# Optimization experiments

Hardware: AMD Instinct MI355X
Metric: run time of the kernel (lower is better)

The kernel has to match this reference:

```python
import jax, jax.numpy as jnp
import numpy as np

B, T, F, H = 512, 64, 256, 1024


def _uniform(key, shape, fan_in):
    stv = 1.0 / np.sqrt(fan_in)
    return jax.random.uniform(key, shape, jnp.float32, -stv, stv)


def setup_inputs() -> dict:
    key = jax.random.key(0)
    ks = jax.random.split(key, 20)
    x = jax.random.normal(ks[0], (B, T, F), jnp.float32)
    mask = (jax.random.uniform(ks[1], (B, T, F)) < 0.8).astype(jnp.float32)
    deltas = jax.random.uniform(ks[2], (B, T, F), jnp.float32) * 5.0
    h0 = jnp.zeros((B, H), jnp.float32)
    return {
        "x": x, "mask": mask, "deltas": deltas, "h0": h0,
        # temp_decay_h: Decay(F -> H), non-diag
        "Wdh": _uniform(ks[3], (H, F), F), "bdh": _uniform(ks[4], (H,), F),
        # temp_decay_x: Decay(F -> F), diag (weight masked with identity)
        "Wdx": _uniform(ks[5], (F, F), F), "bdx": _uniform(ks[6], (F,), F),
        # hist: Linear(H -> F)
        "Wh": _uniform(ks[7], (F, H), H), "bh": _uniform(ks[8], (F,), H),
        "Wfr": _uniform(ks[9], (F, F), F), "bfr": _uniform(ks[10], (F,), F),
        # weight_combine: Linear(2F -> F)
        "Wwc": _uniform(ks[11], (F, 2 * F), 2 * F), "bwc": _uniform(ks[12], (F,), 2 * F),
        # GRUCell(2F, H)
        "Wih": _uniform(ks[13], (3 * H, 2 * F), 2 * F), "bih": _uniform(ks[14], (3 * H,), H),
        "Whh": _uniform(ks[15], (3 * H, H), H), "bhh": _uniform(ks[16], (3 * H,), H),
    }


def _forward(x, mask, deltas, h0, Wdh, bdh, Wdx, bdx, Wh, bh, Wfr, bfr, Wwc, bwc, Wih, bih, Whh, bhh):
    f = x.shape[-1]
    eye = jnp.eye(f, dtype=x.dtype)
    Wdx_diag = Wdx * eye              # diag Decay keeps only diagonal weights
    Wfr_off = Wfr * (1.0 - eye)

    def step(h, xs):
        x_t, m_t, d_t = xs            # each [B, F]
        gamma_h = jnp.exp(-jax.nn.relu(d_t @ Wdh.T + bdh))   # [B, H]
        h = h * gamma_h
        x_h = h @ Wh.T + bh                                   # [B, F]
        x_r = m_t * x_t + (1.0 - m_t) * x_h
        xu = x_r @ Wfr_off.T + bfr
        gamma_x = jnp.exp(-jax.nn.relu(d_t @ Wdx_diag.T + bdx))
        beta = jnp.concatenate([gamma_x, m_t], axis=1) @ Wwc.T + bwc
        x_comb = beta * xu + (1.0 - beta) * x_h
        # MAE on observed entries
        loss_t = jnp.sum(jnp.abs(x_comb - x_t) * m_t) / (jnp.sum(m_t) + 1e-12)
        x_imp_t = m_t * x_t + (1.0 - m_t) * x_comb
        rnn_in = jnp.concatenate([x_imp_t, m_t], axis=1)      # [B, 2F]
        gi = rnn_in @ Wih.T + bih                             # [B, 3H]
        gh = h @ Whh.T + bhh
        i_r, i_z, i_n = jnp.split(gi, 3, axis=1)
        h_r, h_z, h_n = jnp.split(gh, 3, axis=1)
        r = jax.nn.sigmoid(i_r + h_r)
        z = jax.nn.sigmoid(i_z + h_z)
        n = jnp.tanh(i_n + r * h_n)
        h_new = (1.0 - z) * n + z * h
        return h_new, (x_imp_t, x_comb, loss_t)

    xs = (jnp.swapaxes(x, 0, 1), jnp.swapaxes(mask, 0, 1), jnp.swapaxes(deltas, 0, 1))
    h_fin, (imp_t, rec_t, losses) = jax.lax.scan(step, h0, xs)
    x_imp = jnp.swapaxes(imp_t, 0, 1)          # [B, T, F]
    reconstruction = jnp.swapaxes(rec_t, 0, 1) # [B, T, F]
    x_loss = jnp.sum(losses)
    kl_loss = jnp.zeros((), x.dtype)           # non-bayesian path
    return x_imp, reconstruction, h_fin, x_loss, kl_loss


def reference(x, mask, deltas, h0, Wdh, bdh, Wdx, bdx, Wh, bh, Wfr, bfr, Wwc, bwc, Wih, bih, Whh, bhh):
    return _forward(x, mask, deltas, h0, Wdh, bdh, Wdx, bdx, Wh, bh, Wfr, bfr, Wwc, bwc, Wih, bih, Whh, bhh)
```

## Files before the change

### kernel.cpp

```cpp
#include <hip/hip_runtime.h>
#include <hip/hip_bf16.h>

typedef unsigned short u16;
typedef unsigned int u32;
typedef __attribute__((ext_vector_type(4))) float f32x4;
typedef __attribute__((ext_vector_type(8))) short s16x8;

#define OREC 8388608
#define OH 16777216
#define OLOSS 17301504

__device__ __forceinline__ float bf2f(u16 u) {
    union { u32 i; float f; } v; v.i = ((u32)u) << 16; return v.f;
}
__device__ __forceinline__ u16 f2bf(float f) {
    union { float f; u32 i; } v; v.f = f;
    u32 i = v.i;
    u32 r = i + 0x7FFFu + ((i >> 16) & 1u);
    return (u16)(r >> 16);
}
__device__ __forceinline__ float ldin(const void* p, int i, int bf) {
    return bf ? bf2f(((const u16*)p)[i]) : ((const float*)p)[i];
}
__device__ __forceinline__ void stout(void* p, int i, float v, int bf) {
    if (bf) ((u16*)p)[i] = f2bf(v); else ((float*)p)[i] = v;
}

#define ZACC(A) do { \
    _Pragma("unroll") for (int zi = 0; zi < 2; ++zi) \
    _Pragma("unroll") for (int zj = 0; zj < 2; ++zj) \
    _Pragma("unroll") for (int zq = 0; zq < 4; ++zq) A[zi][zj][zq] = 0.f; \
} while (0)

__device__ __forceinline__ void stage_tile(const u16* __restrict__ src, int ld, int row0, int k0,
                                           u16* lds) {
    int t = threadIdx.x;
    int row = t >> 2, seg = t & 3;
    const u16* g = src + (size_t)(row0 + row) * ld + k0 + (seg << 3);
    uint4 v = *(const uint4*)g;
    *(uint4*)&lds[(row << 5) + ((seg ^ (row & 3)) << 3)] = v;
}

__device__ __forceinline__ void gemm_loop(const u16* __restrict__ A, int lda,
                                          const u16* __restrict__ W, int ldw,
                                          int K, int m0, int n0,
                                          u16* lA, u16* lB, f32x4 acc[2][2]) {
    int lane = threadIdx.x & 63;
    int wid = threadIdx.x >> 6;
    int wr = wid >> 1, wc = wid & 1;
    int lrow = lane & 15, lseg = lane >> 4;
    int sw = (lseg ^ (lrow & 3)) << 3;
    for (int k0 = 0; k0 < K; k0 += 32) {
        __syncthreads();
        stage_tile(A, lda, m0, k0, lA);
        stage_tile(W, ldw, n0, k0, lB);
        __syncthreads();
        s16x8 af[2], bg[2];
#pragma unroll
        for (int i = 0; i < 2; i++) {
            int r = (wr << 5) + (i << 4) + lrow;
            af[i] = *(const s16x8*)&lA[(r << 5) + sw];
            int c = (wc << 5) + (i << 4) + lrow;
            bg[i] = *(const s16x8*)&lB[(c << 5) + sw];
        }
#pragma unroll
        for (int i = 0; i < 2; i++)
#pragma unroll
            for (int j = 0; j < 2; j++)
                acc[i][j] = __builtin_amdgcn_mfma_f32_16x16x32_bf16(af[i], bg[j], acc[i][j], 0, 0, 0);
    }
}

__global__ void k_zero(int* flag, float* lossN, float* lossD) {
    if (threadIdx.x == 0) *flag = 0;
    if (threadIdx.x < 64) { lossN[threadIdx.x] = 0.f; lossD[threadIdx.x] = 0.f; }
}

__global__ void k_detect(const u32* __restrict__ w, int* flag) {
    int gid = blockIdx.x * 256 + threadIdx.x;
    int found = 0;
    for (int i = gid; i < (1 << 20); i += 65536) {
        if ((w[i] & 0xFFFFu) == 0x3F80u) found = 1;
    }
    if (found) atomicOr(flag, 1);
}

__global__ void k_cvt_bf(const void* __restrict__ src, u16* __restrict__ dst, int n,
                         const int* __restrict__ flagp) {
    int bf = *flagp;
    for (int i = blockIdx.x * 256 + threadIdx.x; i < n; i += gridDim.x * 256)
        dst[i] = bf ? ((const u16*)src)[i] : f2bf(((const float*)src)[i]);
}

__global__ void k_packW2(const void* __restrict__ Wih, const void* __restrict__ Whh,
                         u16* __restrict__ W2B, const int* __restrict__ flagp) {
    int bf = *flagp;
    int c = blockIdx.x;
    int k0 = threadIdx.x;
#pragma unroll
    for (int j = 0; j < 6; ++j) {
        int k = k0 + (j << 8);
        float v = (k < 512) ? ldin(Wih, c * 512 + k, bf)
                            : ldin(Whh, c * 1024 + (k - 512), bf);
        W2B[(size_t)c * 1536 + k] = f2bf(v);
    }
}

__global__ void k_cvt_biases(const void* __restrict__ bdh, const void* __restrict__ bdx,
                             const void* __restrict__ bh, const void* __restrict__ bfr,
                             const void* __restrict__ bwc, const void* __restrict__ bih,
                             const void* __restrict__ bhh, float* __restrict__ dst,
                             const int* __restrict__ flagp) {
    int bf = *flagp;
    int i = blockIdx.x * 256 + threadIdx.x;
    const void* src; int off;
    if (i < 1024) { src = bdh; off = 0; }
    else if (i < 1280) { src = bdx; off = 1024; }
    else if (i < 1536) { src = bh; off = 1280; }
    else if (i < 1792) { src = bfr; off = 1536; }
    else if (i < 2048) { src = bwc; off = 1792; }
    else if (i < 5120) { src = bih; off = 2048; }
    else { src = bhh; off = 5120; }
    dst[i] = ldin(src, i - off, bf);
}

__global__ void k_fixup(u16* __restrict__ WfrB, float* __restrict__ wdxd,
                        const void* __restrict__ Wdx, const int* __restrict__ flagp) {
    int f = threadIdx.x;
    int bf = *flagp;
    WfrB[f * 256 + f] = 0;
    wdxd[f] = ldin(Wdx, f * 257, bf);
}

__global__ void k_pack(const void* __restrict__ x, const void* __restrict__ deltas,
                       const void* __restrict__ mask, const int* __restrict__ flagp,
                       const float* __restrict__ wdxd, const float* __restrict__ bdx,
                       u16* __restrict__ dbf_all, u16* __restrict__ A2_all,
                       u16* __restrict__ xbf_all) {
    int bf = *flagp;
    for (int idx = blockIdx.x * 256 + threadIdx.x; idx < 8388608; idx += gridDim.x * 256) {
        int f = idx & 255;
        int bt = idx >> 8;
        int b = bt >> 6, t = bt & 63;
        float d = ldin(deltas, idx, bf);
        float m = ldin(mask, idx, bf);
        float xv = ldin(x, idx, bf);
        int r = t * 512 + b;
        dbf_all[(r << 8) + f] = f2bf(d);
        xbf_all[(r << 8) + f] = f2bf(xv);
        float gx = __expf(-fmaxf(d * wdxd[f] + bdx[f], 0.f));
        A2_all[(r << 9) + f] = f2bf(gx);
        A2_all[(r << 9) + 256 + f] = f2bf(m);
    }
}

__global__ __launch_bounds__(256) void k_gammaH(const u16* __restrict__ dbf_all,
                                                const u16* __restrict__ WdhB,
                                                const float* __restrict__ bdh,
                                                u16* __restrict__ gammaH) {
    __shared__ u16 lA[2048], lB[2048];
    int m0 = blockIdx.x << 6, n0 = blockIdx.y << 6;
    f32x4 acc[2][2]; ZACC(acc);
    gemm_loop(dbf_all, 256, WdhB, 256, 256, m0, n0, lA, lB, acc);
    int lane = threadIdx.x & 63, wid = threadIdx.x >> 6;
    int wr = wid >> 1, wc = wid & 1;
    int rq = (lane >> 4) << 2, cc = lane & 15;
#pragma unroll
    for (int i = 0; i < 2; i++)
#pragma unroll
        for (int j = 0; j < 2; j++)
#pragma unroll
            for (int q = 0; q < 4; q++) {
                int gr = m0 + (wr << 5) + (i << 4) + rq + q;
                int gc = n0 + (wc << 5) + (j << 4) + cc;
                gammaH[((size_t)gr << 10) + gc] = f2bf(__expf(-fmaxf(acc[i][j][q] + bdh[gc], 0.f)));
            }
}

__global__ __launch_bounds__(256) void k_beta(const u16* __restrict__ A2_all,
                                              const u16* __restrict__ WwcB,
                                              const float* __restrict__ bwc,
                                              u16* __restrict__ betaB) {
    __shared__ u16 lA[2048], lB[2048];
    int m0 = blockIdx.x << 6, n0 = blockIdx.y << 6;
    f32x4 acc[2][2]; ZACC(acc);
    gemm_loop(A2_all, 512, WwcB, 512, 512, m0, n0, lA, lB, acc);
    int lane = threadIdx.x & 63, wid = threadIdx.x >> 6;
    int wr = wid >> 1, wc = wid & 1;
    int rq = (lane >> 4) << 2, cc = lane & 15;
#pragma unroll
    for (int i = 0; i < 2; i++)
#pragma unroll
        for (int j = 0; j < 2; j++)
#pragma unroll
            for (int q = 0; q < 4; q++) {
                int gr = m0 + (wr << 5) + (i << 4) + rq + q;
                int gc = n0 + (wc << 5) + (j << 4) + cc;
                betaB[((size_t)gr << 8) + gc] = f2bf(acc[i][j][q] + bwc[gc]);
            }
}

__global__ void k_hinit(const void* __restrict__ h0, const int* __restrict__ flagp,
                        const u16* __restrict__ gammaH, u16* __restrict__ A3x) {
    int bf = *flagp;
    int i = blockIdx.x * 256 + threadIdx.x;
    float g = bf2f(gammaH[i]);
    float hv = ldin(h0, i, bf) * g;
    int r = i >> 10, c = i & 1023;
    A3x[(size_t)r * 2560 + 512 + c] = f2bf(hv);
}

__global__ __launch_bounds__(512) void k_step1(
    u16* __restrict__ A3x, u16* __restrict__ pbufB,
    const u16* __restrict__ WhB, const u16* __restrict__ WfrB,
    const u16* __restrict__ W2B,
    const float* __restrict__ biases, const u16* __restrict__ betaB,
    const u16* __restrict__ xbf_all, const u16* __restrict__ A2_all,
    int t, const int* __restrict__ flagp,
    void* __restrict__ out, float* __restrict__ lossN, float* __restrict__ lossD) {
    __shared__ u16 smem[20736];
    __shared__ float redN[8], redD[8];
    int tid = threadIdx.x, bid = blockIdx.x;
    int lane = tid & 63, w = tid >> 6;
    int lrow = lane & 15, lseg = lane >> 4;
    int hsel = 512 + ((t & 1) << 10);

    if (bid < 32) {
        u16* lH = smem;
        u16* lXR = smem + 16512;
        int m0 = bid << 4;
        int c0 = w << 5;
        int bf = *flagp;
        {
            int row = tid >> 5;
            int colb = (tid & 31) << 3;
            const u16* src = A3x + (size_t)(m0 + row) * 2560 + hsel;
#pragma unroll
            for (int j = 0; j < 4; ++j) {
                int off = colb + (j << 8);
                *(uint4*)&lH[row * 1032 + off] = *(const uint4*)&src[off];
            }
        }
        __syncthreads();

        f32x4 acc[2] = {};
#pragma unroll 4
        for (int k0 = 0; k0 < 1024; k0 += 32) {
            int kk = k0 + (lseg << 3);
            s16x8 a = *(const s16x8*)&lH[lrow * 1032 + kk];
#pragma unroll
            for (int j = 0; j < 2; ++j) {
                s16x8 b = *(const s16x8*)&WhB[((size_t)(c0 + (j << 4) + lrow) << 10) + kk];
                acc[j] = __builtin_amdgcn_mfma_f32_16x16x32_bf16(a, b, acc[j], 0, 0, 0);
            }
        }

        float xhr[2][4], mvr[2][4], xvr[2][4];
#pragma unroll
        for (int j = 0; j < 2; ++j) {
            int gc = c0 + (j << 4) + lrow;
            float bhc = biases[1280 + gc];
#pragma unroll
            for (int q = 0; q < 4; ++q) {
                int r = (lseg << 2) + q;
                int gr = m0 + r;
                float v = acc[j][q] + bhc;
                size_t rbase = (size_t)t * 512 + gr;
                float mv = bf2f(A2_all[(rbase << 9) + 256 + gc]);
                float xv = bf2f(xbf_all[(rbase << 8) + gc]);
                xhr[j][q] = v; mvr[j][q] = mv; xvr[j][q] = xv;
                lXR[r * 264 + gc] = f2bf(mv * xv + (1.f - mv) * v);
            }
        }
        __syncthreads();

        f32x4 accF[2] = {};
#pragma unroll
        for (int k0 = 0; k0 < 256; k0 += 32) {
            int kk = k0 + (lseg << 3);
            s16x8 a = *(const s16x8*)&lXR[lrow * 264 + kk];
#pragma unroll
            for (int j = 0; j < 2; ++j) {
                s16x8 b = *(const s16x8*)&WfrB[((size_t)(c0 + (j << 4) + lrow) << 8) + kk];
                accF[j] = __builtin_amdgcn_mfma_f32_16x16x32_bf16(a, b, accF[j], 0, 0, 0);
            }
        }

        float ln = 0.f, ldn = 0.f;
#pragma unroll
        for (int j = 0; j < 2; ++j) {
            int gc = c0 + (j << 4) + lrow;
            float bfrc = biases[1536 + gc];
#pragma unroll
            for (int q = 0; q < 4; ++q) {
                int r = (lseg << 2) + q;
                int gr = m0 + r;
                float xu = accF[j][q] + bfrc;
                float beta = bf2f(betaB[(((size_t)t * 512 + gr) << 8) + gc]);
                float xc = beta * xu + (1.f - beta) * xhr[j][q];
                int gidx = (gr << 14) + (t << 8) + gc;
                float mv = mvr[j][q], xv = xvr[j][q];
                stout(out, OREC + gidx, xc, bf);
                float xi = mv * xv + (1.f - mv) * xc;
                stout(out, gidx, xi, bf);
                A3x[(size_t)gr * 2560 + gc] = f2bf(xi);
                A3x[(size_t)gr * 2560 + 256 + gc] = f2bf(mv);
                ln += fabsf(xc - xv) * mv;
                ldn += mv;
            }
        }
        for (int o = 32; o > 0; o >>= 1) { ln += __shfl_down(ln, o); ldn += __shfl_down(ldn, o); }
        if (lane == 0) { redN[w] = ln; redD[w] = ldn; }
        __syncthreads();
        if (tid == 0) {
            float sn = 0.f, sd = 0.f;
#pragma unroll
            for (int i = 0; i < 8; ++i) { sn += redN[i]; sd += redD[i]; }
            atomicAdd(&lossN[t], sn);
            atomicAdd(&lossD[t], sd);
        }
    } else {
        u16* lds = smem;
        int g = bid - 32;
        int kz = g >> 8;
        int gs = g & 255;
        int nt = ((gs & 7) << 1) | ((gs >> 3) & 1);
        int m0 = (gs >> 4) << 5, n0 = nt << 6;
        int bcol = 512 + (kz << 9);
        int acol = hsel + (kz << 9);
        int wr = w & 1, wc = w >> 1;

        int br0 = tid >> 2, sg0 = tid & 3;
        int g0 = br0 >> 6;
        const u16* Bg0 = W2B + (size_t)(g0 * 1024 + n0 + (br0 & 63)) * 1536 + bcol + (sg0 << 3);
        int isB1 = (tid < 256), isA1 = (tid >= 256 && tid < 384);
        int br1 = 128 + (tid >> 2);
        const u16* Bg1 = W2B + (size_t)(2048 + n0 + (br1 & 63)) * 1536 + bcol + (sg0 << 3);
        int ar1 = (tid - 256) >> 2, sg1 = tid & 3;
        const u16* Ag1 = A3x + (size_t)(m0 + ar1) * 2560 + acol + (sg1 << 3);

        uint4 p0, p1;
        auto issue = [&](int it) {
            int ko = it << 5;
            p0 = *(const uint4*)(Bg0 + ko);
            if (isB1) p1 = *(const uint4*)(Bg1 + ko);
            else if (isA1) p1 = *(const uint4*)(Ag1 + ko);
        };
        auto store = [&](u16* lb) {
            *(uint4*)&lb[br0 * 40 + (sg0 << 3)] = p0;
            if (isB1) *(uint4*)&lb[br1 * 40 + (sg0 << 3)] = p1;
            else if (isA1) *(uint4*)&lb[7680 + ar1 * 40 + (sg1 << 3)] = p1;
        };

        f32x4 aR = {0.f, 0.f, 0.f, 0.f}, aZ = {0.f, 0.f, 0.f, 0.f}, aN = {0.f, 0.f, 0.f, 0.f};
        issue(0);
        store(lds);
        __syncthreads();
        int cur = 0;
#pragma unroll 1
        for (int it = 0; it < 16; ++it) {
            if (it + 1 < 16) issue(it + 1);
            u16* lc = lds + (cur ? 8960 : 0);
            s16x8 a = *(const s16x8*)&lc[7680 + ((wr << 4) + lrow) * 40 + (lseg << 3)];
            int bro = ((wc << 4) + lrow) * 40 + (lseg << 3);
            s16x8 b0 = *(const s16x8*)&lc[bro];
            aR = __builtin_amdgcn_mfma_f32_16x16x32_bf16(a, b0, aR, 0, 0, 0);
            s16x8 b1 = *(const s16x8*)&lc[2560 + bro];
            aZ = __builtin_amdgcn_mfma_f32_16x16x32_bf16(a, b1, aZ, 0, 0, 0);
            s16x8 b2 = *(const s16x8*)&lc[5120 + bro];
            aN = __builtin_amdgcn_mfma_f32_16x16x32_bf16(a, b2, aN, 0, 0, 0);
            if (it + 1 < 16) store(lds + (cur ? 0 : 8960));
            __syncthreads();
            cur ^= 1;
        }

        size_t kzoff = (size_t)kz * 1572864;
        int colR = n0 + (wc << 4) + lrow;
#pragma unroll
        for (int q = 0; q < 4; ++q) {
            int row = m0 + (wr << 4) + (lseg << 2) + q;
            size_t o = ((size_t)row << 10) + colR;
            pbufB[kzoff + o] = f2bf(aR[q]);
            pbufB[kzoff + 524288 + o] = f2bf(aZ[q]);
            pbufB[kzoff + 1048576 + o] = f2bf(aN[q]);
        }
    }
}

__global__ __launch_bounds__(256) void k_step2(
    u16* __restrict__ A3x, const u16* __restrict__ W2B,
    const u16* __restrict__ pbufB, const float* __restrict__ biases,
    const u16* __restrict__ gammaH, int t, void* __restrict__ out,
    const int* __restrict__ flagp) {
    __shared__ u16 lds[16640];
    int tid = threadIdx.x, bid = blockIdx.x;
    int nt = ((bid & 7) << 1) | ((bid >> 3) & 1);
    int m0 = (bid >> 4) << 4, n0 = nt << 6;
    int lane = tid & 63, w = tid >> 6;
    int lrow = lane & 15, lseg = lane >> 4;

    int r0 = tid >> 2, sg = tid & 3;
    const u16* BgR = W2B + (size_t)(n0 + r0) * 1536 + (sg << 3);
    const u16* BgZ = W2B + (size_t)(1024 + n0 + r0) * 1536 + (sg << 3);
    const u16* BgN = W2B + (size_t)(2048 + n0 + r0) * 1536 + (sg << 3);
    int isA = (tid < 64);
    const u16* Ag = A3x + (size_t)(m0 + r0) * 2560 + (sg << 3);

    uint4 pR, pZ, pN, pA;
    auto issue = [&](int it) {
        int ko = it << 5;
        pR = *(const uint4*)(BgR + ko);
        pZ = *(const uint4*)(BgZ + ko);
        pN = *(const uint4*)(BgN + ko);
        if (isA) pA = *(const uint4*)(Ag + ko);
    };
    auto store = [&](u16* lb) {
        int o = r0 * 40 + (sg << 3);
        *(uint4*)&lb[o] = pR;
        *(uint4*)&lb[2560 + o] = pZ;
        *(uint4*)&lb[5120 + o] = pN;
        if (isA) *(uint4*)&lb[7680 + o] = pA;
    };

    f32x4 aR = {0.f, 0.f, 0.f, 0.f}, aZ = {0.f, 0.f, 0.f, 0.f}, aN = {0.f, 0.f, 0.f, 0.f};
    issue(0);
    store(lds);
    __syncthreads();
    int cur = 0;
#pragma unroll 1
    for (int it = 0; it < 16; ++it) {
        if (it + 1 < 16) issue(it + 1);
        u16* lc = lds + (cur ? 8320 : 0);
        s16x8 a = *(const s16x8*)&lc[7680 + lrow * 40 + (lseg << 3)];
        int bro = ((w << 4) + lrow) * 40 + (lseg << 3);
        s16x8 b0 = *(const s16x8*)&lc[bro];
        aR = __builtin_amdgcn_mfma_f32_16x16x32_bf16(a, b0, aR, 0, 0, 0);
        s16x8 b1 = *(const s16x8*)&lc[2560 + bro];
        aZ = __builtin_amdgcn_mfma_f32_16x16x32_bf16(a, b1, aZ, 0, 0, 0);
        s16x8 b2 = *(const s16x8*)&lc[5120 + bro];
        aN = __builtin_amdgcn_mfma_f32_16x16x32_bf16(a, b2, aN, 0, 0, 0);
        if (it + 1 < 16) store(lds + (cur ? 0 : 8320));
        __syncthreads();
        cur ^= 1;
    }

    int bf = *flagp;
    int hsel = 512 + ((t & 1) << 10);
    int nseg = 512 + (((t + 1) & 1) << 10);
    int last = (t == 63);
    int colR = n0 + (w << 4) + lrow;
    float bRi = biases[2048 + colR] + biases[5120 + colR];
    float bZi = biases[3072 + colR] + biases[6144 + colR];
    float bNi = biases[4096 + colR];
    float bNh = biases[7168 + colR];
#pragma unroll
    for (int q = 0; q < 4; ++q) {
        int row = m0 + (lseg << 2) + q;
        size_t o = ((size_t)row << 10) + colR;
        float pRv = bf2f(pbufB[o]) + bf2f(pbufB[1572864 + o]);
        float pZv = bf2f(pbufB[524288 + o]) + bf2f(pbufB[2097152 + o]);
        float pNv = bf2f(pbufB[1048576 + o]) + bf2f(pbufB[2621440 + o]);
        float rr = 1.f / (1.f + expf(-(aR[q] + pRv + bRi)));
        float zz = 1.f / (1.f + expf(-(aZ[q] + pZv + bZi)));
        float nn = tanhf(aN[q] + bNi + rr * (pNv + bNh));
        float hp = bf2f(A3x[(size_t)row * 2560 + hsel + colR]);
        float hv = (1.f - zz) * nn + zz * hp;
        if (!last) {
            hv *= bf2f(gammaH[(((size_t)(t + 1) * 512 + row) << 10) + colR]);
            A3x[(size_t)row * 2560 + nseg + colR] = f2bf(hv);
        } else {
            stout(out, OH + (row << 10) + colR, hv, bf);
        }
    }
}

__global__ void k_loss(const float* __restrict__ lossN, const float* __restrict__ lossD,
                       void* __restrict__ out, const int* __restrict__ flagp) {
    int t = threadIdx.x;
    float v = lossN[t] / (lossD[t] + 1e-12f);
    for (int o = 32; o > 0; o >>= 1) v += __shfl_down(v, o);
    if (t == 0) {
        int bf = *flagp;
        stout(out, OLOSS, v, bf);
        stout(out, OLOSS + 1, 0.f, bf);
    }
}

extern "C" void kernel_launch(void* const* d_in, const int* in_sizes, int n_in,
                              void* d_out, int out_size, void* d_ws, size_t ws_size,
                              hipStream_t stream) {
    (void)in_sizes; (void)n_in; (void)out_size; (void)ws_size;
    const void* x = d_in[0];
    const void* mask = d_in[1];
    const void* deltas = d_in[2];
    const void* h0 = d_in[3];
    const void* Wdh = d_in[4];  const void* bdh = d_in[5];
    const void* Wdx = d_in[6];  const void* bdx = d_in[7];
    const void* Wh = d_in[8];   const void* bh = d_in[9];
    const void* Wfr = d_in[10]; const void* bfr = d_in[11];
    const void* Wwc = d_in[12]; const void* bwc = d_in[13];
    const void* Wih = d_in[14]; const void* bih = d_in[15];
    const void* Whh = d_in[16]; const void* bhh = d_in[17];

    char* cur = (char*)d_ws;
    auto carve = [&](size_t bytes) -> char* {
        char* p = cur; cur += (bytes + 255) & ~(size_t)255; return p;
    };
    int* flag = (int*)carve(sizeof(int));
    float* lossN = (float*)carve(64 * 4);
    float* lossD = (float*)carve(64 * 4);
    float* wdxd = (float*)carve(256 * 4);
    float* biasesF = (float*)carve(8192 * 4);
    u16* WdhB = (u16*)carve(262144 * 2);
    u16* WhB = (u16*)carve(262144 * 2);
    u16* WfrB = (u16*)carve(65536 * 2);
    u16* WwcB = (u16*)carve(131072 * 2);
    u16* W2B = (u16*)carve((size_t)4718592 * 2);
    u16* A3x = (u16*)carve((size_t)512 * 2560 * 2);
    u16* pbufB = (u16*)carve((size_t)6 * 524288 * 2);
    u16* dbf_all = (u16*)carve((size_t)8388608 * 2);
    u16* A2_all = (u16*)carve((size_t)16777216 * 2);
    u16* xbf_all = (u16*)carve((size_t)8388608 * 2);
    u16* gammaH_all = (u16*)carve((size_t)33554432 * 2);
    u16* betaB = (u16*)carve((size_t)8388608 * 2);

    float* bdhF = biasesF;
    float* bdxF = biasesF + 1024;

    k_zero<<<1, 64, 0, stream>>>(flag, lossN, lossD);
    k_detect<<<256, 256, 0, stream>>>((const u32*)mask, flag);
    k_cvt_bf<<<1024, 256, 0, stream>>>(Wdh, WdhB, 262144, flag);
    k_cvt_bf<<<1024, 256, 0, stream>>>(Wh, WhB, 262144, flag);
    k_cvt_bf<<<256, 256, 0, stream>>>(Wfr, WfrB, 65536, flag);
    k_cvt_bf<<<512, 256, 0, stream>>>(Wwc, WwcB, 131072, flag);
    k_packW2<<<3072, 256, 0, stream>>>(Wih, Whh, W2B, flag);
    k_cvt_biases<<<32, 256, 0, stream>>>(bdh, bdx, bh, bfr, bwc, bih, bhh, biasesF, flag);
    k_fixup<<<1, 256, 0, stream>>>(WfrB, wdxd, Wdx, flag);

    k_pack<<<8192, 256, 0, stream>>>(x, deltas, mask, flag, wdxd, bdxF,
                                     dbf_all, A2_all, xbf_all);
    k_gammaH<<<dim3(512, 16), 256, 0, stream>>>(dbf_all, WdhB, bdhF, gammaH_all);
    k_beta<<<dim3(512, 4), 256, 0, stream>>>(A2_all, WwcB, biasesF + 1792, betaB);
    k_hinit<<<2048, 256, 0, stream>>>(h0, flag, gammaH_all, A3x);

    for (int t = 0; t < 64; ++t) {
        k_step1<<<544, 512, 0, stream>>>(A3x, pbufB, WhB, WfrB, W2B, biasesF, betaB,
                                         xbf_all, A2_all, t, flag, d_out, lossN, lossD);
        k_step2<<<512, 256, 0, stream>>>(A3x, W2B, pbufB, biasesF, gammaH_all, t,
                                         d_out, flag);
    }
    k_loss<<<1, 64, 0, stream>>>(lossN, lossD, d_out, flag);
}
```

Before: 2.818 ms.

## Deepen GEMM prefetch to two stages, hoist epilogue loads, vectorize pack

The two recurrent GEMM kernels now keep two register sets of global tile loads in flight, so each load has two iterations to arrive instead of one. k_step2 also issues its epilogue reads (partial sums, previous h, next gamma) before the main loop so their latency overlaps the MFMA work. The pack kernel handles four elements per thread with vector loads and stores. The extra register sets raise register pressure and could lower occupancy.

```diff
diff --git a/kernel.cpp b/kernel.cpp
--- a/kernel.cpp
+++ b/kernel.cpp
@@ -138,19 +138,41 @@
                        u16* __restrict__ dbf_all, u16* __restrict__ A2_all,
                        u16* __restrict__ xbf_all) {
     int bf = *flagp;
-    for (int idx = blockIdx.x * 256 + threadIdx.x; idx < 8388608; idx += gridDim.x * 256) {
+    int base = (blockIdx.x * 256 + threadIdx.x) << 2;
+    for (int idx = base; idx < 8388608; idx += (gridDim.x << 10)) {
+        float d[4], m[4], xv[4];
+        if (bf) {
+            ushort4 dv = *(const ushort4*)&((const u16*)deltas)[idx];
+            ushort4 mv = *(const ushort4*)&((const u16*)mask)[idx];
+            ushort4 xw = *(const ushort4*)&((const u16*)x)[idx];
+            d[0] = bf2f(dv.x); d[1] = bf2f(dv.y); d[2] = bf2f(dv.z); d[3] = bf2f(dv.w);
+            m[0] = bf2f(mv.x); m[1] = bf2f(mv.y); m[2] = bf2f(mv.z); m[3] = bf2f(mv.w);
+            xv[0] = bf2f(xw.x); xv[1] = bf2f(xw.y); xv[2] = bf2f(xw.z); xv[3] = bf2f(xw.w);
+        } else {
+            float4 dv = *(const float4*)&((const float*)deltas)[idx];
+            float4 mv = *(const float4*)&((const float*)mask)[idx];
+            float4 xw = *(const float4*)&((const float*)x)[idx];
+            d[0] = dv.x; d[1] = dv.y; d[2] = dv.z; d[3] = dv.w;
+            m[0] = mv.x; m[1] = mv.y; m[2] = mv.z; m[3] = mv.w;
+            xv[0] = xw.x; xv[1] = xw.y; xv[2] = xw.z; xv[3] = xw.w;
+        }
         int f = idx & 255;
         int bt = idx >> 8;
         int b = bt >> 6, t = bt & 63;
-        float d = ldin(deltas, idx, bf);
-        float m = ldin(mask, idx, bf);
-        float xv = ldin(x, idx, bf);
         int r = t * 512 + b;
-        dbf_all[(r << 8) + f] = f2bf(d);
-        xbf_all[(r << 8) + f] = f2bf(xv);
-        float gx = __expf(-fmaxf(d * wdxd[f] + bdx[f], 0.f));
-        A2_all[(r << 9) + f] = f2bf(gx);
-        A2_all[(r << 9) + 256 + f] = f2bf(m);
+        ushort4 db, xb, gb, mb;
+        float g0 = __expf(-fmaxf(d[0] * wdxd[f] + bdx[f], 0.f));
+        float g1 = __expf(-fmaxf(d[1] * wdxd[f + 1] + bdx[f + 1], 0.f));
+        float g2 = __expf(-fmaxf(d[2] * wdxd[f + 2] + bdx[f + 2], 0.f));
+        float g3 = __expf(-fmaxf(d[3] * wdxd[f + 3] + bdx[f + 3], 0.f));
+        db.x = f2bf(d[0]); db.y = f2bf(d[1]); db.z = f2bf(d[2]); db.w = f2bf(d[3]);
+        xb.x = f2bf(xv[0]); xb.y = f2bf(xv[1]); xb.z = f2bf(xv[2]); xb.w = f2bf(xv[3]);
+        gb.x = f2bf(g0); gb.y = f2bf(g1); gb.z = f2bf(g2); gb.w = f2bf(g3);
+        mb.x = f2bf(m[0]); mb.y = f2bf(m[1]); mb.z = f2bf(m[2]); mb.w = f2bf(m[3]);
+        *(ushort4*)&dbf_all[(r << 8) + f] = db;
+        *(ushort4*)&xbf_all[(r << 8) + f] = xb;
+        *(ushort4*)&A2_all[(r << 9) + f] = gb;
+        *(ushort4*)&A2_all[(r << 9) + 256 + f] = mb;
     }
 }
 
@@ -339,27 +361,31 @@
         int ar1 = (tid - 256) >> 2, sg1 = tid & 3;
         const u16* Ag1 = A3x + (size_t)(m0 + ar1) * 2560 + acol + (sg1 << 3);
 
-        uint4 p0, p1;
-        auto issue = [&](int it) {
+        uint4 q0, q1, r0v, r1v;
+        auto issueP = [&](uint4& a, uint4& b, int it) {
             int ko = it << 5;
-            p0 = *(const uint4*)(Bg0 + ko);
-            if (isB1) p1 = *(const uint4*)(Bg1 + ko);
-            else if (isA1) p1 = *(const uint4*)(Ag1 + ko);
+            a = *(const uint4*)(Bg0 + ko);
+            if (isB1) b = *(const uint4*)(Bg1 + ko);
+            else if (isA1) b = *(const uint4*)(Ag1 + ko);
         };
-        auto store = [&](u16* lb) {
-            *(uint4*)&lb[br0 * 40 + (sg0 << 3)] = p0;
-            if (isB1) *(uint4*)&lb[br1 * 40 + (sg0 << 3)] = p1;
-            else if (isA1) *(uint4*)&lb[7680 + ar1 * 40 + (sg1 << 3)] = p1;
+        auto storeP = [&](uint4& a, uint4& b, u16* lb) {
+            *(uint4*)&lb[br0 * 40 + (sg0 << 3)] = a;
+            if (isB1) *(uint4*)&lb[br1 * 40 + (sg0 << 3)] = b;
+            else if (isA1) *(uint4*)&lb[7680 + ar1 * 40 + (sg1 << 3)] = b;
         };
 
         f32x4 aR = {0.f, 0.f, 0.f, 0.f}, aZ = {0.f, 0.f, 0.f, 0.f}, aN = {0.f, 0.f, 0.f, 0.f};
-        issue(0);
-        store(lds);
+        issueP(q0, q1, 0);
+        storeP(q0, q1, lds);
+        issueP(r0v, r1v, 1);
         __syncthreads();
         int cur = 0;
 #pragma unroll 1
         for (int it = 0; it < 16; ++it) {
-            if (it + 1 < 16) issue(it + 1);
+            if (it + 2 < 16) {
+                if (it & 1) issueP(r0v, r1v, it + 2);
+                else issueP(q0, q1, it + 2);
+            }
             u16* lc = lds + (cur ? 8960 : 0);
             s16x8 a = *(const s16x8*)&lc[7680 + ((wr << 4) + lrow) * 40 + (lseg << 3)];
             int bro = ((wc << 4) + lrow) * 40 + (lseg << 3);
@@ -369,7 +395,10 @@
             aZ = __builtin_amdgcn_mfma_f32_16x16x32_bf16(a, b1, aZ, 0, 0, 0);
             s16x8 b2 = *(const s16x8*)&lc[5120 + bro];
             aN = __builtin_amdgcn_mfma_f32_16x16x32_bf16(a, b2, aN, 0, 0, 0);
-            if (it + 1 < 16) store(lds + (cur ? 0 : 8960));
+            if (it + 1 < 16) {
+                if (it & 1) storeP(q0, q1, lds + (cur ? 0 : 8960));
+                else storeP(r0v, r1v, lds + (cur ? 0 : 8960));
+            }
             __syncthreads();
             cur ^= 1;
         }
@@ -399,6 +428,23 @@
     int lane = tid & 63, w = tid >> 6;
     int lrow = lane & 15, lseg = lane >> 4;
 
+    int hsel = 512 + ((t & 1) << 10);
+    int nseg = 512 + (((t + 1) & 1) << 10);
+    int last = (t == 63);
+    int colR = n0 + (w << 4) + lrow;
+
+    float pRv[4], pZv[4], pNv[4], hpv[4], gmv[4];
+#pragma unroll
+    for (int q = 0; q < 4; ++q) {
+        int row = m0 + (lseg << 2) + q;
+        size_t o = ((size_t)row << 10) + colR;
+        pRv[q] = bf2f(pbufB[o]) + bf2f(pbufB[1572864 + o]);
+        pZv[q] = bf2f(pbufB[524288 + o]) + bf2f(pbufB[2097152 + o]);
+        pNv[q] = bf2f(pbufB[1048576 + o]) + bf2f(pbufB[2621440 + o]);
+        hpv[q] = bf2f(A3x[(size_t)row * 2560 + hsel + colR]);
+        gmv[q] = last ? 1.f : bf2f(gammaH[(((size_t)(t + 1) * 512 + row) << 10) + colR]);
+    }
+
     int r0 = tid >> 2, sg = tid & 3;
     const u16* BgR = W2B + (size_t)(n0 + r0) * 1536 + (sg << 3);
     const u16* BgZ = W2B + (size_t)(1024 + n0 + r0) * 1536 + (sg << 3);
@@ -406,30 +452,34 @@
     int isA = (tid < 64);
     const u16* Ag = A3x + (size_t)(m0 + r0) * 2560 + (sg << 3);
 
-    uint4 pR, pZ, pN, pA;
-    auto issue = [&](int it) {
+    uint4 qR, qZ, qN, qA, rR, rZ, rN, rA;
+    auto issueP = [&](uint4& vR, uint4& vZ, uint4& vN, uint4& vA, int it) {
         int ko = it << 5;
-        pR = *(const uint4*)(BgR + ko);
-        pZ = *(const uint4*)(BgZ + ko);
-        pN = *(const uint4*)(BgN + ko);
-        if (isA) pA = *(const uint4*)(Ag + ko);
+        vR = *(const uint4*)(BgR + ko);
+        vZ = *(const uint4*)(BgZ + ko);
+        vN = *(const uint4*)(BgN + ko);
+        if (isA) vA = *(const uint4*)(Ag + ko);
     };
-    auto store = [&](u16* lb) {
+    auto storeP = [&](uint4& vR, uint4& vZ, uint4& vN, uint4& vA, u16* lb) {
         int o = r0 * 40 + (sg << 3);
-        *(uint4*)&lb[o] = pR;
-        *(uint4*)&lb[2560 + o] = pZ;
-        *(uint4*)&lb[5120 + o] = pN;
-        if (isA) *(uint4*)&lb[7680 + o] = pA;
+        *(uint4*)&lb[o] = vR;
+        *(uint4*)&lb[2560 + o] = vZ;
+        *(uint4*)&lb[5120 + o] = vN;
+        if (isA) *(uint4*)&lb[7680 + o] = vA;
     };
 
     f32x4 aR = {0.f, 0.f, 0.f, 0.f}, aZ = {0.f, 0.f, 0.f, 0.f}, aN = {0.f, 0.f, 0.f, 0.f};
-    issue(0);
-    store(lds);
+    issueP(qR, qZ, qN, qA, 0);
+    storeP(qR, qZ, qN, qA, lds);
+    issueP(rR, rZ, rN, rA, 1);
     __syncthreads();
     int cur = 0;
 #pragma unroll 1
     for (int it = 0; it < 16; ++it) {
-        if (it + 1 < 16) issue(it + 1);
+        if (it + 2 < 16) {
+            if (it & 1) issueP(rR, rZ, rN, rA, it + 2);
+            else issueP(qR, qZ, qN, qA, it + 2);
+        }
         u16* lc = lds + (cur ? 8320 : 0);
         s16x8 a = *(const s16x8*)&lc[7680 + lrow * 40 + (lseg << 3)];
         int bro = ((w << 4) + lrow) * 40 + (lseg << 3);
@@ -439,16 +489,15 @@
         aZ = __builtin_amdgcn_mfma_f32_16x16x32_bf16(a, b1, aZ, 0, 0, 0);
         s16x8 b2 = *(const s16x8*)&lc[5120 + bro];
         aN = __builtin_amdgcn_mfma_f32_16x16x32_bf16(a, b2, aN, 0, 0, 0);
-        if (it + 1 < 16) store(lds + (cur ? 0 : 8320));
+        if (it + 1 < 16) {
+            if (it & 1) storeP(qR, qZ, qN, qA, lds + (cur ? 0 : 8320));
+            else storeP(rR, rZ, rN, rA, lds + (cur ? 0 : 8320));
+        }
         __syncthreads();
         cur ^= 1;
     }
 
     int bf = *flagp;
-    int hsel = 512 + ((t & 1) << 10);
-    int nseg = 512 + (((t + 1) & 1) << 10);
-    int last = (t == 63);
-    int colR = n0 + (w << 4) + lrow;
     float bRi = biases[2048 + colR] + biases[5120 + colR];
     float bZi = biases[3072 + colR] + biases[6144 + colR];
     float bNi = biases[4096 + colR];
@@ -456,17 +505,12 @@
 #pragma unroll
     for (int q = 0; q < 4; ++q) {
         int row = m0 + (lseg << 2) + q;
-        size_t o = ((size_t)row << 10) + colR;
-        float pRv = bf2f(pbufB[o]) + bf2f(pbufB[1572864 + o]);
-        float pZv = bf2f(pbufB[524288 + o]) + bf2f(pbufB[2097152 + o]);
-        float pNv = bf2f(pbufB[1048576 + o]) + bf2f(pbufB[2621440 + o]);
-        float rr = 1.f / (1.f + expf(-(aR[q] + pRv + bRi)));
-        float zz = 1.f / (1.f + expf(-(aZ[q] + pZv + bZi)));
-        float nn = tanhf(aN[q] + bNi + rr * (pNv + bNh));
-        float hp = bf2f(A3x[(size_t)row * 2560 + hsel + colR]);
-        float hv = (1.f - zz) * nn + zz * hp;
+        float rr = 1.f / (1.f + expf(-(aR[q] + pRv[q] + bRi)));
+        float zz = 1.f / (1.f + expf(-(aZ[q] + pZv[q] + bZi)));
+        float nn = tanhf(aN[q] + bNi + rr * (pNv[q] + bNh));
+        float hv = (1.f - zz) * nn + zz * hpv[q];
         if (!last) {
-            hv *= bf2f(gammaH[(((size_t)(t + 1) * 512 + row) << 10) + colR]);
+            hv *= gmv[q];
             A3x[(size_t)row * 2560 + nseg + colR] = f2bf(hv);
         } else {
             stout(out, OH + (row << 10) + colR, hv, bf);
```

After: 2.876 ms. +2.1%, slower.
